# Kernel optimization log

Measured on AMD Instinct MI355X. Metric: run time of the kernel, lower is better.

## Reference

```python
import jax, jax.numpy as jnp
import numpy as np

NUM_TOKENS = 4096
IN_FEATURES = 4096
OUT_FEATURES = 4096
MAX_PACKED = 4


def setup_inputs() -> dict:
    key = jax.random.key(0)
    k1, k2, k3 = jax.random.split(key, 3)
    x = jax.random.normal(k1, (NUM_TOKENS, IN_FEATURES), dtype=jnp.float32)
    weight_stacked = jax.random.normal(
        k2, (MAX_PACKED, OUT_FEATURES, IN_FEATURES), dtype=jnp.float32) * 0.02
    indices = jax.random.randint(k3, (NUM_TOKENS,), 0, MAX_PACKED, dtype=jnp.int32)
    return {"x": x, "weight_stacked": weight_stacked, "indices": indices}


def reference(x, weight_stacked, indices):
    # apply_swap: outputs[t] = x[t] @ weight_stacked[indices[t]].T
    # Grouped-GEMM expressed as E dense GEMMs with masked combine
    # (E = max_packed is a small static constant).
    E = weight_stacked.shape[0]
    out = jnp.zeros((x.shape[0], weight_stacked.shape[1]), dtype=x.dtype)
    for e in range(E):
        sel = (indices == e)[:, None].astype(x.dtype)  # [T,1]
        out = out + sel * jnp.einsum('ti,oi->to', x, weight_stacked[e])
    return out
```

## Files before the change

kernel.cpp:

```cpp
#include <hip/hip_runtime.h>

#define T 4096
#define K 4096
#define O 4096
#define E 4
#define BK 64
#define MAXT128 35

typedef __attribute__((ext_vector_type(8))) short bf16x8;
typedef __attribute__((ext_vector_type(4))) float f32x4;

__device__ __forceinline__ unsigned short f2bf(float f) {
  unsigned int u = __float_as_uint(f);
  u += 0x7fffu + ((u >> 16) & 1u);
  return (unsigned short)(u >> 16);
}

__global__ void build_meta(const int* __restrict__ idx, int* __restrict__ perm,
                           int* __restrict__ meta, int4* __restrict__ t256,
                           int4* __restrict__ t128, int4* __restrict__ sched) {
  const int wave = threadIdx.x >> 6;
  const int lane = threadIdx.x & 63;
  __shared__ int s_off[E + 1];
  __shared__ int rtE[20], rtP[20], rtC[20];
  __shared__ int r_sh;
  int total = 0;
  for (int t0 = 0; t0 < T; t0 += 64)
    total += __popcll(__ballot(idx[t0 + lane] == wave));
  if (lane == 0) s_off[wave + 1] = total;
  __syncthreads();
  if (threadIdx.x == 0) {
    s_off[0] = 0;
    for (int e = 0; e < E; e++) s_off[e + 1] += s_off[e];
  }
  __syncthreads();
  int base = s_off[wave];
  const unsigned long long below = (1ull << lane) - 1ull;
  for (int t0 = 0; t0 < T; t0 += 64) {
    int e = idx[t0 + lane];
    unsigned long long m = __ballot(e == wave);
    if (e == wave) perm[base + __popcll(m & below)] = t0 + lane;
    base += __popcll(m);
  }
  if (threadIdx.x == 0) {
    int n = 0;
    for (int e = 0; e < E; e++) {
      int s = s_off[e], c = s_off[e + 1] - s;
      for (int ro = 0; ro < c; ro += 256) {
        rtE[n] = e; rtP[n] = s + ro; rtC[n] = (c - ro) < 256 ? (c - ro) : 256; n++;
      }
    }
    r_sh = n;
    meta[0] = n * 16;
    int n1 = 0;
    for (int e = 0; e < E; e++) {
      int s = s_off[e], c = s_off[e + 1] - s;
      for (int ro = 0; ro < c; ro += 128)
        t128[n1++] = make_int4(e, s + ro, (c - ro) < 128 ? (c - ro) : 128, 0);
    }
    for (; n1 < MAXT128; n1++) t128[n1] = make_int4(-1, 0, 0, 0);
  }
  __syncthreads();
  const int r = r_sh;
  for (int i = threadIdx.x; i < 16 * r; i += 256)
    t256[i] = make_int4(rtE[i >> 4], rtP[i >> 4], rtC[i >> 4], (i & 15) * 256);
  {
    const int b = threadIdx.x;
    const int ru = r - 16;
    const int xcd = b & 7, s = b >> 3;
    const int rt_ = 4 * (xcd >> 1) + (s >> 3);
    const int nt_ = 8 * (xcd & 1) + (s & 7);
    sched[b * 3 + 0] = make_int4(rt_ * 16 + nt_, 0, 16, 0);
    int sgi = 1, u0 = b * ru, u1 = u0 + ru;
    while (u0 < u1) {
      int tI = 256 + (u0 >> 4), q0 = u0 & 15;
      int avail = 16 - q0, want = u1 - u0;
      int take = want < avail ? want : avail;
      sched[b * 3 + sgi] = make_int4(tI, q0, take, 0);
      sgi++; u0 += take;
    }
    for (; sgi < 3; sgi++) sched[b * 3 + sgi] = make_int4(-1, 0, 0, 0);
  }
}

__global__ void zero_rem(const int* __restrict__ meta, const int4* __restrict__ t256,
                         const int* __restrict__ perm, float* __restrict__ out) {
  const int ntiles = meta[0];
  const int tI = 256 + (int)blockIdx.x / 16;
  if (tI >= ntiles) return;
  const int4 td = t256[tI];
  const int rt = (blockIdx.x & 15) * 16 + ((int)threadIdx.x >> 4);
  if (rt >= td.z) return;
  float4* p = (float4*)(out + (size_t)perm[td.y + rt] * O + td.w) + (threadIdx.x & 15) * 4;
  const float4 z = {0.f, 0.f, 0.f, 0.f};
  p[0] = z; p[1] = z; p[2] = z; p[3] = z;
}

__global__ void convert_kernel(const float4* __restrict__ w4, const float* __restrict__ x,
                               const int* __restrict__ perm,
                               ushort4* __restrict__ wb4, ushort4* __restrict__ xg4) {
  const size_t NW4 = (size_t)E * O * K / 4;
  const size_t NX4 = (size_t)T * K / 4;
  const size_t stride = (size_t)gridDim.x * blockDim.x;
  for (size_t i = (size_t)blockIdx.x * blockDim.x + threadIdx.x; i < NW4 + NX4; i += stride) {
    if (i < NW4) {
      float4 v = w4[i];
      wb4[i] = make_ushort4(f2bf(v.x), f2bf(v.y), f2bf(v.z), f2bf(v.w));
    } else {
      size_t j = i - NW4;
      int p = (int)(j >> 10);
      int c = (int)(j & 1023);
      float4 v = *((const float4*)(x + (size_t)perm[p] * K) + c);
      xg4[j] = make_ushort4(f2bf(v.x), f2bf(v.y), f2bf(v.z), f2bf(v.w));
    }
  }
}

__global__ __launch_bounds__(512, 2)
void gemm8p(const unsigned short* __restrict__ xg, const unsigned short* __restrict__ wbb,
            const int* __restrict__ perm, const int4* __restrict__ t256,
            const int4* __restrict__ sched, float* __restrict__ out) {
  __shared__ unsigned short lds[65536];
  const int bid = blockIdx.x;
  const int tid = threadIdx.x;
  const int wid = tid >> 6, lane = tid & 63;
  const int wr = wid >> 2, wc = wid & 3;
  const int kc4 = lane >> 4;
  unsigned short* ldsw = &lds[wid * 512];

#define GLL(gp, lp) __builtin_amdgcn_global_load_lds( \
    (const __attribute__((address_space(1))) void*)(gp), \
    (__attribute__((address_space(3))) void*)(lp), 16, 0, 0)
#define STAGE_A(bo, kh, ko) do { \
    GLL(srcA0 + (ko) + (kh) * 32, ldsw + (bo) + (kh) * 8192); \
    GLL(srcA1 + (ko) + (kh) * 32, ldsw + (bo) + (kh) * 8192 + 4096); \
  } while (0)
#define STAGE_B(bo, kh, ko) do { \
    GLL(srcB0 + (ko) + (kh) * 32, ldsw + (bo) + 16384 + (kh) * 8192); \
    GLL(srcB1 + (ko) + (kh) * 32, ldsw + (bo) + 16384 + (kh) * 8192 + 4096); \
  } while (0)
#define LOADA(dst, bo, ks, mh) do { _Pragma("unroll") \
    for (int mi = 0; mi < 4; ++mi) \
      dst[mi] = *(const bf16x8*)&lds[(bo) + (ks) * 8192 + aoff[mh][mi]]; } while (0)
#define LOADB(dst, bo, ks) do { _Pragma("unroll") \
    for (int ni = 0; ni < 4; ++ni) \
      dst[ni] = *(const bf16x8*)&lds[(bo) + 16384 + (ks) * 8192 + boff[ni]]; } while (0)
#define MFMA16(A, B, mh) do { _Pragma("unroll") \
    for (int mi = 0; mi < 4; ++mi) _Pragma("unroll") \
      for (int ni = 0; ni < 4; ++ni) \
        acc[(mh) * 4 + mi][ni] = __builtin_amdgcn_mfma_f32_16x16x32_bf16( \
            A[mi], B[ni], acc[(mh) * 4 + mi][ni], 0, 0, 0); } while (0)
#define BAR() do { __builtin_amdgcn_s_barrier(); asm volatile("" ::: "memory"); } while (0)
#define VM0() asm volatile("s_waitcnt vmcnt(0)" ::: "memory")
#define PRIO1() __builtin_amdgcn_s_setprio(1)
#define PRIO0() __builtin_amdgcn_s_setprio(0)

#define KTILE(C, X, koe) do { \
    const int ko = (koe); \
    STAGE_A(X, 0, ko); STAGE_B(X, 0, ko); \
    STAGE_A(X, 1, ko); STAGE_B(X, 1, ko); \
    LOADA(afP, C, 0, 0); LOADB(bfP, C, 0); \
    PRIO1(); MFMA16(afP, bfP, 0); PRIO0(); \
    LOADA(afQ, C, 0, 1); \
    PRIO1(); MFMA16(afQ, bfP, 1); PRIO0(); \
    LOADA(afP, C, 1, 0); LOADB(bfQ, C, 1); \
    PRIO1(); MFMA16(afP, bfQ, 0); PRIO0(); \
    LOADA(afQ, C, 1, 1); \
    PRIO1(); MFMA16(afQ, bfQ, 1); PRIO0(); \
    VM0(); BAR(); \
  } while (0)

  int aoff[2][4], boff[4];
#pragma unroll
  for (int mh = 0; mh < 2; ++mh)
#pragma unroll
    for (int mi = 0; mi < 4; ++mi) {
      int r = wr * 128 + mh * 64 + mi * 16 + (lane & 15);
      aoff[mh][mi] = (((r >> 1) << 3) + (((((r & 1) << 2) | kc4)) ^ ((r >> 1) & 7))) * 8;
    }
#pragma unroll
  for (int ni = 0; ni < 4; ++ni) {
    int r = wc * 64 + ni * 16 + (lane & 15);
    boff[ni] = (((r >> 1) << 3) + (((((r & 1) << 2) | kc4)) ^ ((r >> 1) & 7))) * 8;
  }

  for (int sg = 0; sg < 3; ++sg) {
    const int4 sd = sched[bid * 3 + sg];
    if (sd.x < 0) break;
    const int4 td = t256[sd.x];
    const int e = td.x, p0 = td.y, rc = td.z, n0 = td.w;
    const int kt0 = sd.y << 2;
    const int nt = sd.z << 2;

    const unsigned short *srcA0, *srcA1, *srcB0, *srcB1;
    {
      const unsigned short* wB = wbb + (size_t)e * O * K + (size_t)n0 * K;
      int s0 = tid, s1 = 512 + tid;
      int b0 = s0 >> 3, v0 = (s0 & 7) ^ (b0 & 7);
      int r0 = b0 * 2 + (v0 >> 2), c0 = v0 & 3;
      int b1 = s1 >> 3, v1 = (s1 & 7) ^ (b1 & 7);
      int r1 = b1 * 2 + (v1 >> 2), c1 = v1 & 3;
      int ra0 = r0 < rc ? r0 : rc - 1;
      int ra1 = r1 < rc ? r1 : rc - 1;
      srcA0 = xg + (size_t)(p0 + ra0) * K + c0 * 8;
      srcA1 = xg + (size_t)(p0 + ra1) * K + c1 * 8;
      srcB0 = wB + (size_t)r0 * K + c0 * 8;
      srcB1 = wB + (size_t)r1 * K + c1 * 8;
    }

    f32x4 acc[8][4] = {};
    bf16x8 afP[4], afQ[4], bfP[4], bfQ[4];

    const int kb = kt0 << 6;
    STAGE_A(0, 0, kb); STAGE_B(0, 0, kb);
    STAGE_A(0, 1, kb); STAGE_B(0, 1, kb);
    VM0(); BAR();

    for (int tp = 0; tp < nt; tp += 2) {
      KTILE(0, 32768, ((tp + 1 < nt ? tp + 1 : tp) + kt0) << 6);
      KTILE(32768, 0, ((tp + 2 < nt ? tp + 2 : tp + 1) + kt0) << 6);
    }

    if (sd.z == 16) {
#pragma unroll
      for (int mh = 0; mh < 2; ++mh)
#pragma unroll
        for (int mi = 0; mi < 4; ++mi) {
          const int rbase = wr * 128 + mh * 64 + mi * 16 + (lane >> 4) * 4;
#pragma unroll
          for (int reg = 0; reg < 4; ++reg) {
            const int pr = rbase + reg;
            if (pr < rc) {
              float* orow = out + (size_t)perm[p0 + pr] * O + n0 + wc * 64 + (lane & 15);
#pragma unroll
              for (int ni = 0; ni < 4; ++ni) orow[ni * 16] = acc[mh * 4 + mi][ni][reg];
            }
          }
        }
    } else {
#pragma unroll
      for (int mh = 0; mh < 2; ++mh)
#pragma unroll
        for (int mi = 0; mi < 4; ++mi) {
          const int rbase = wr * 128 + mh * 64 + mi * 16 + (lane >> 4) * 4;
#pragma unroll
          for (int reg = 0; reg < 4; ++reg) {
            const int pr = rbase + reg;
            if (pr < rc) {
              float* orow = out + (size_t)perm[p0 + pr] * O + n0 + wc * 64 + (lane & 15);
#pragma unroll
              for (int ni = 0; ni < 4; ++ni)
                unsafeAtomicAdd(&orow[ni * 16], acc[mh * 4 + mi][ni][reg]);
            }
          }
        }
    }
  }
}

__global__ __launch_bounds__(256)
void gemm_fb(const float* __restrict__ xf, const float* __restrict__ wf,
             const int* __restrict__ perm, const int4* __restrict__ tiles,
             float* __restrict__ out) {
  __shared__ unsigned short lds_a[128 * 64];
  __shared__ unsigned short lds_b[128 * 64];
  const int4 td = tiles[blockIdx.x];
  if (td.x < 0) return;
  const int e = td.x, p0 = td.y, rc = td.z;
  const int n0 = blockIdx.y * 128;
  const int wave = threadIdx.x >> 6, lane = threadIdx.x & 63;
  const int wr = wave >> 1, wc = wave & 1;
  f32x4 acc[4][4] = {};
  const float* wf_base = wf + (size_t)e * O * K + (size_t)n0 * K;
  for (int k0 = 0; k0 < K; k0 += 64) {
    if (k0) __syncthreads();
#pragma unroll
    for (int i = 0; i < 8; i++) {
      int l4 = i * 256 + (int)threadIdx.x;
      int row = l4 >> 4;
      int c4 = (l4 & 15) << 2;
      int ra = row < rc ? row : (rc - 1);
      const float4 va = *(const float4*)(xf + (size_t)perm[p0 + ra] * K + k0 + c4);
      *(ushort4*)&lds_a[row * 64 + c4] = make_ushort4(f2bf(va.x), f2bf(va.y), f2bf(va.z), f2bf(va.w));
      const float4 vb = *(const float4*)(wf_base + (size_t)row * K + k0 + c4);
      *(ushort4*)&lds_b[row * 64 + c4] = make_ushort4(f2bf(vb.x), f2bf(vb.y), f2bf(vb.z), f2bf(vb.w));
    }
    __syncthreads();
#pragma unroll
    for (int ks = 0; ks < 2; ks++) {
      bf16x8 a2[4], b2[4];
#pragma unroll
      for (int mi = 0; mi < 4; mi++)
        a2[mi] = *(const bf16x8*)&lds_a[(wr * 64 + mi * 16 + (lane & 15)) * 64 + ks * 32 + (lane >> 4) * 8];
#pragma unroll
      for (int ni = 0; ni < 4; ni++)
        b2[ni] = *(const bf16x8*)&lds_b[(wc * 64 + ni * 16 + (lane & 15)) * 64 + ks * 32 + (lane >> 4) * 8];
#pragma unroll
      for (int mi = 0; mi < 4; mi++)
#pragma unroll
        for (int ni = 0; ni < 4; ni++)
          acc[mi][ni] = __builtin_amdgcn_mfma_f32_16x16x32_bf16(a2[mi], b2[ni], acc[mi][ni], 0, 0, 0);
    }
  }
#pragma unroll
  for (int mi = 0; mi < 4; mi++) {
    const int rb = wr * 64 + mi * 16 + (lane >> 4) * 4;
#pragma unroll
    for (int reg = 0; reg < 4; reg++) {
      const int rt = rb + reg;
      if (rt < rc) {
        float* orow = out + (size_t)perm[p0 + rt] * O + n0 + wc * 64 + (lane & 15);
#pragma unroll
        for (int ni = 0; ni < 4; ni++) orow[ni * 16] = acc[mi][ni][reg];
      }
    }
  }
}

extern "C" void kernel_launch(void* const* d_in, const int* in_sizes, int n_in,
                              void* d_out, int out_size, void* d_ws, size_t ws_size,
                              hipStream_t stream) {
  const float* x = (const float*)d_in[0];
  const float* w = (const float*)d_in[1];
  const int* idx = (const int*)d_in[2];
  float* out = (float*)d_out;
  char* ws = (char*)d_ws;

  int* perm = (int*)ws;
  int* meta = (int*)(ws + 16384);
  int4* t256 = (int4*)(ws + 16640);
  int4* t128 = (int4*)(ws + 22528);
  int4* sched = (int4*)(ws + 24576);
  unsigned short* xg = (unsigned short*)(ws + 65536);
  unsigned short* wb = xg + (size_t)T * K;
  const size_t need = 65536 + (size_t)T * K * 2 + (size_t)E * O * K * 2;

  build_meta<<<1, 256, 0, stream>>>(idx, perm, meta, t256, t128, sched);
  if (ws_size >= need) {
    zero_rem<<<768, 256, 0, stream>>>(meta, t256, perm, out);
    convert_kernel<<<2048, 256, 0, stream>>>((const float4*)w, x, perm,
                                             (ushort4*)wb, (ushort4*)xg);
    gemm8p<<<256, 512, 0, stream>>>(xg, wb, perm, t256, sched, out);
  } else {
    gemm_fb<<<dim3(MAXT128, 32), 256, 0, stream>>>(x, w, perm, t128, out);
  }
}
```

Baseline: 284.5 us.

## Restructure GEMM k-tile into four barrier-synchronised quadrant phases and split convert loops

The GEMM inner k-tile now runs in four phases. Each phase loads A/B fragments for both k-slices of one output quadrant and interleaves the global-to-LDS staging with explicit lgkmcnt waits and extra barriers, so that the waves' MFMA bursts line up. The convert kernel is split into two separate grid-stride loops for weights and activations, removing a per-element branch, and its grid is doubled. The extra barriers add sync overhead and could stall waves, while A fragments are reloaded twice per tile, which raises LDS traffic.

```diff
diff --git a/kernel.cpp b/kernel.cpp
--- a/kernel.cpp
+++ b/kernel.cpp
@@ -102,17 +102,16 @@
   const size_t NW4 = (size_t)E * O * K / 4;
   const size_t NX4 = (size_t)T * K / 4;
   const size_t stride = (size_t)gridDim.x * blockDim.x;
-  for (size_t i = (size_t)blockIdx.x * blockDim.x + threadIdx.x; i < NW4 + NX4; i += stride) {
-    if (i < NW4) {
-      float4 v = w4[i];
-      wb4[i] = make_ushort4(f2bf(v.x), f2bf(v.y), f2bf(v.z), f2bf(v.w));
-    } else {
-      size_t j = i - NW4;
-      int p = (int)(j >> 10);
-      int c = (int)(j & 1023);
-      float4 v = *((const float4*)(x + (size_t)perm[p] * K) + c);
-      xg4[j] = make_ushort4(f2bf(v.x), f2bf(v.y), f2bf(v.z), f2bf(v.w));
-    }
+  const size_t t0 = (size_t)blockIdx.x * blockDim.x + threadIdx.x;
+  for (size_t i = t0; i < NW4; i += stride) {
+    float4 v = w4[i];
+    wb4[i] = make_ushort4(f2bf(v.x), f2bf(v.y), f2bf(v.z), f2bf(v.w));
+  }
+  for (size_t j = t0; j < NX4; j += stride) {
+    int p = (int)(j >> 10);
+    int c = (int)(j & 1023);
+    float4 v = *((const float4*)(x + (size_t)perm[p] * K) + c);
+    xg4[j] = make_ushort4(f2bf(v.x), f2bf(v.y), f2bf(v.z), f2bf(v.w));
   }
 }
 
@@ -139,34 +138,50 @@
     GLL(srcB0 + (ko) + (kh) * 32, ldsw + (bo) + 16384 + (kh) * 8192); \
     GLL(srcB1 + (ko) + (kh) * 32, ldsw + (bo) + 16384 + (kh) * 8192 + 4096); \
   } while (0)
-#define LOADA(dst, bo, ks, mh) do { _Pragma("unroll") \
-    for (int mi = 0; mi < 4; ++mi) \
-      dst[mi] = *(const bf16x8*)&lds[(bo) + (ks) * 8192 + aoff[mh][mi]]; } while (0)
-#define LOADB(dst, bo, ks) do { _Pragma("unroll") \
-    for (int ni = 0; ni < 4; ++ni) \
-      dst[ni] = *(const bf16x8*)&lds[(bo) + 16384 + (ks) * 8192 + boff[ni]]; } while (0)
-#define MFMA16(A, B, mh) do { _Pragma("unroll") \
-    for (int mi = 0; mi < 4; ++mi) _Pragma("unroll") \
-      for (int ni = 0; ni < 4; ++ni) \
-        acc[(mh) * 4 + mi][ni] = __builtin_amdgcn_mfma_f32_16x16x32_bf16( \
-            A[mi], B[ni], acc[(mh) * 4 + mi][ni], 0, 0, 0); } while (0)
+#define LOADA2(bo, mh) do { _Pragma("unroll") \
+    for (int ks = 0; ks < 2; ++ks) _Pragma("unroll") \
+      for (int mi = 0; mi < 4; ++mi) \
+        afk[ks][mi] = *(const bf16x8*)&lds[(bo) + ks * 8192 + aoff[mh][mi]]; } while (0)
+#define LOADB2(bo, nb) do { _Pragma("unroll") \
+    for (int ks = 0; ks < 2; ++ks) _Pragma("unroll") \
+      for (int j = 0; j < 2; ++j) \
+        bfk[ks][j] = *(const bf16x8*)&lds[(bo) + 16384 + ks * 8192 + boff[(nb) + j]]; } while (0)
+#define MF16(mib, nib) do { _Pragma("unroll") \
+    for (int ks = 0; ks < 2; ++ks) _Pragma("unroll") \
+      for (int mi = 0; mi < 4; ++mi) _Pragma("unroll") \
+        for (int j = 0; j < 2; ++j) \
+          acc[(mib) + mi][(nib) + j] = __builtin_amdgcn_mfma_f32_16x16x32_bf16( \
+              afk[ks][mi], bfk[ks][j], acc[(mib) + mi][(nib) + j], 0, 0, 0); } while (0)
 #define BAR() do { __builtin_amdgcn_s_barrier(); asm volatile("" ::: "memory"); } while (0)
+#define LGKM0() asm volatile("s_waitcnt lgkmcnt(0)" ::: "memory")
+#define LGKM8() asm volatile("s_waitcnt lgkmcnt(8)" ::: "memory")
 #define VM0() asm volatile("s_waitcnt vmcnt(0)" ::: "memory")
 #define PRIO1() __builtin_amdgcn_s_setprio(1)
 #define PRIO0() __builtin_amdgcn_s_setprio(0)
 
 #define KTILE(C, X, koe) do { \
     const int ko = (koe); \
+     \
+    LOADA2(C, 0); LOADB2(C, 0); \
     STAGE_A(X, 0, ko); STAGE_B(X, 0, ko); \
+    LGKM8(); BAR(); LGKM0(); \
+    PRIO1(); MF16(0, 0); PRIO0(); \
+    BAR(); \
+     \
+    LOADA2(C, 1); \
     STAGE_A(X, 1, ko); STAGE_B(X, 1, ko); \
-    LOADA(afP, C, 0, 0); LOADB(bfP, C, 0); \
-    PRIO1(); MFMA16(afP, bfP, 0); PRIO0(); \
-    LOADA(afQ, C, 0, 1); \
-    PRIO1(); MFMA16(afQ, bfP, 1); PRIO0(); \
-    LOADA(afP, C, 1, 0); LOADB(bfQ, C, 1); \
-    PRIO1(); MFMA16(afP, bfQ, 0); PRIO0(); \
-    LOADA(afQ, C, 1, 1); \
-    PRIO1(); MFMA16(afQ, bfQ, 1); PRIO0(); \
+    BAR(); LGKM0(); \
+    PRIO1(); MF16(4, 0); PRIO0(); \
+    BAR(); \
+     \
+    LOADB2(C, 2); \
+    BAR(); LGKM0(); \
+    PRIO1(); MF16(4, 2); PRIO0(); \
+    BAR(); \
+     \
+    LOADA2(C, 0); \
+    BAR(); LGKM0(); \
+    PRIO1(); MF16(0, 2); PRIO0(); \
     VM0(); BAR(); \
   } while (0)
 
@@ -209,7 +224,7 @@
     }
 
     f32x4 acc[8][4] = {};
-    bf16x8 afP[4], afQ[4], bfP[4], bfQ[4];
+    bf16x8 afk[2][4], bfk[2][2];
 
     const int kb = kt0 << 6;
     STAGE_A(0, 0, kb); STAGE_B(0, 0, kb);
@@ -220,6 +235,7 @@
       KTILE(0, 32768, ((tp + 1 < nt ? tp + 1 : tp) + kt0) << 6);
       KTILE(32768, 0, ((tp + 2 < nt ? tp + 2 : tp + 1) + kt0) << 6);
     }
+    VM0();
 
     if (sd.z == 16) {
 #pragma unroll
@@ -338,7 +354,7 @@
   build_meta<<<1, 256, 0, stream>>>(idx, perm, meta, t256, t128, sched);
   if (ws_size >= need) {
     zero_rem<<<768, 256, 0, stream>>>(meta, t256, perm, out);
-    convert_kernel<<<2048, 256, 0, stream>>>((const float4*)w, x, perm,
+    convert_kernel<<<4096, 256, 0, stream>>>((const float4*)w, x, perm,
                                              (ushort4*)wb, (ushort4*)xg);
     gemm8p<<<256, 512, 0, stream>>>(xg, wb, perm, t256, sched, out);
   } else {
```

After: 291.8 us. 2.6% more time.
